# Optimization experiments

Measured on AMD Instinct MI355X. Metric: run time of the kernel, lower is better.

## Reference

```python
import jax, jax.numpy as jnp
import numpy as np

B, S, D, H = 4, 2048, 1024, 16
DK = D // H  # 64


def setup_inputs() -> dict:
    key = jax.random.key(0)
    ks = jax.random.split(key, 11)
    scale = 1.0 / np.sqrt(D)
    inp = {
        "query": jax.random.normal(ks[0], (B, S, D), jnp.float32),
        "key": jax.random.normal(ks[1], (B, S, D), jnp.float32),
        "value": jax.random.normal(ks[2], (B, S, D), jnp.float32),
        "Wq": jax.random.normal(ks[3], (D, D), jnp.float32) * scale,
        "bq": jnp.zeros((D,), jnp.float32),
        "Wk": jax.random.normal(ks[4], (D, D), jnp.float32) * scale,
        "bk": jnp.zeros((D,), jnp.float32),
        "Wv": jax.random.normal(ks[5], (D, D), jnp.float32) * scale,
        "bv": jnp.zeros((D,), jnp.float32),
        "Wo": jax.random.normal(ks[6], (D, D), jnp.float32) * scale,
        "bo": jnp.zeros((D,), jnp.float32),
    }
    return inp


def reference(query, key, value, Wq, bq, Wk, bk, Wv, bv, Wo, bo):
    # Projections: torch Linear computes x @ W.T + b; here W is stored as (in, out)
    def split_heads(x):
        return x.reshape(B, S, H, DK).transpose(0, 2, 1, 3)  # [B,H,S,DK]

    Q = split_heads(query @ Wq + bq)
    K = split_heads(key @ Wk + bk)
    V = split_heads(value @ Wv + bv)

    scores = jnp.einsum("bhqd,bhkd->bhqk", Q, K) / jnp.sqrt(jnp.float32(DK))
    attn = jax.nn.softmax(scores, axis=-1)  # [B,H,S,S]
    ctx = jnp.einsum("bhqk,bhkd->bhqd", attn, V)
    ctx = ctx.transpose(0, 2, 1, 3).reshape(B, S, D)
    return ctx @ Wo + bo
```

## Files before the change

kernel.cpp:

```cpp
#include <hip/hip_runtime.h>
#include <hip/hip_bf16.h>
#include <cstdint>

#define DEV __device__ __forceinline__

typedef __bf16 bf16x8 __attribute__((ext_vector_type(8)));
typedef float f32x4 __attribute__((ext_vector_type(4)));
typedef unsigned short u16;
typedef unsigned short u16x8 __attribute__((ext_vector_type(8)));
typedef unsigned short u16x4 __attribute__((ext_vector_type(4)));

#if defined(__has_builtin) && __has_builtin(__builtin_amdgcn_exp2f)
#define EXP2F(x) __builtin_amdgcn_exp2f(x)
#else
#define EXP2F(x) exp2f(x)
#endif

static constexpr float QSCALE = 0.125f * 1.44269504088896340736f;

DEV u16 f2bf(float f) {
  uint32_t x = __builtin_bit_cast(uint32_t, f);
  x += 0x7fffu + ((x >> 16) & 1u);
  return (u16)(x >> 16);
}

DEV u16x4 pack4(float a, float b, float c, float d) {
  union { __hip_bfloat162 h[2]; u16x4 u; } r;
  r.h[0] = __float22bfloat162_rn(make_float2(a, b));
  r.h[1] = __float22bfloat162_rn(make_float2(c, d));
  return r.u;
}

DEV u16x8 cvt8(const float* p) {
  const float4 v0 = *(const float4*)p;
  const float4 v1 = *(const float4*)(p + 4);
  union { __hip_bfloat162 h[4]; u16x8 u; } r;
  r.h[0] = __float22bfloat162_rn(make_float2(v0.x, v0.y));
  r.h[1] = __float22bfloat162_rn(make_float2(v0.z, v0.w));
  r.h[2] = __float22bfloat162_rn(make_float2(v1.x, v1.y));
  r.h[3] = __float22bfloat162_rn(make_float2(v1.z, v1.w));
  return r.u;
}

DEV f32x4 mfma16(bf16x8 a, bf16x8 b, f32x4 c) {
  return __builtin_amdgcn_mfma_f32_16x16x32_bf16(a, b, c, 0, 0, 0);
}

DEV void gll16(const void* g, const void* l) {
  __builtin_amdgcn_global_load_lds(
      (const __attribute__((address_space(1))) uint32_t*)g,
      (__attribute__((address_space(3))) uint32_t*)l, 16, 0, 0);
}

__global__ __launch_bounds__(256) void cvt_kernel(
    const float* __restrict__ X0, const float* __restrict__ X1,
    const float* __restrict__ X2, u16* __restrict__ Y0,
    u16* __restrict__ Y1, u16* __restrict__ Y2) {
  const float* X = (blockIdx.z == 0) ? X0 : (blockIdx.z == 1) ? X1 : X2;
  u16* Y = (blockIdx.z == 0) ? Y0 : (blockIdx.z == 1) ? Y1 : Y2;
  const size_t i = ((size_t)blockIdx.x * 256 + threadIdx.x) * 8;
  *(u16x8*)(Y + i) = cvt8(X + i);
}

__global__ __launch_bounds__(256) void wtrans_kernel(
    const float* __restrict__ W0, const float* __restrict__ W1,
    const float* __restrict__ W2, const float* __restrict__ W3,
    u16* __restrict__ T0, u16* __restrict__ T1,
    u16* __restrict__ T2, u16* __restrict__ T3) {
  const float* W = (blockIdx.z == 0) ? W0 : (blockIdx.z == 1) ? W1 : (blockIdx.z == 2) ? W2 : W3;
  u16* T = (blockIdx.z == 0) ? T0 : (blockIdx.z == 1) ? T1 : (blockIdx.z == 2) ? T2 : T3;
  __shared__ float tile[32][33];
  const int tid = threadIdx.x;
  const int r = tid >> 3, c0 = (tid & 7) * 4;
  const float4 v = *(const float4*)(W + (size_t)(blockIdx.y * 32 + r) * 1024 + blockIdx.x * 32 + c0);
  tile[r][c0 + 0] = v.x; tile[r][c0 + 1] = v.y; tile[r][c0 + 2] = v.z; tile[r][c0 + 3] = v.w;
  __syncthreads();
  u16x4 o = pack4(tile[c0 + 0][r], tile[c0 + 1][r], tile[c0 + 2][r], tile[c0 + 3][r]);
  *(u16x4*)(T + (size_t)(blockIdx.x * 32 + r) * 1024 + blockIdx.y * 32 + c0) = o;
}

__global__ __launch_bounds__(512) void gemm_qkv_kernel(
    const u16* __restrict__ X0, const u16* __restrict__ X1,
    const u16* __restrict__ X2, const u16* __restrict__ W0t,
    const u16* __restrict__ W1t, const u16* __restrict__ W2t,
    const float* __restrict__ b0, const float* __restrict__ b1,
    const float* __restrict__ b2, u16* __restrict__ O0,
    u16* __restrict__ O1, u16* __restrict__ O2) {
  __shared__ u16 As[128 * 32];
  __shared__ u16 Bs[128 * 32];
  const int z = blockIdx.z;
  const u16* X = (z == 0) ? X0 : (z == 1) ? X1 : X2;
  const u16* Wt = (z == 0) ? W0t : (z == 1) ? W1t : W2t;
  const float* bias = (z == 0) ? b0 : (z == 1) ? b1 : b2;
  u16* O = (z == 0) ? O0 : (z == 1) ? O1 : O2;
  const float scale = (z == 0) ? QSCALE : 1.0f;

  const int tid = threadIdx.x;
  const int w = tid >> 6, lane = tid & 63, ln = lane & 15, quad = lane >> 4;
  const int wm = w >> 1, wn = w & 1;
  const int bm = blockIdx.y * 128, bn = blockIdx.x * 128;

  f32x4 acc[2][4];
#pragma unroll
  for (int i = 0; i < 2; i++)
#pragma unroll
    for (int j = 0; j < 4; j++) acc[i][j] = f32x4{0.f, 0.f, 0.f, 0.f};

  const int lrow = w * 16 + (lane >> 2);
  const u16* ga = X + (size_t)(bm + lrow) * 1024 + (lane & 3) * 8;
  const u16* gb = Wt + (size_t)(bn + lrow) * 1024 + (lane & 3) * 8;
  const u16* lA = As + w * 512;
  const u16* lB = Bs + w * 512;

  for (int kt = 0; kt < 32; ++kt) {
    __syncthreads();
    gll16(ga + kt * 32, lA);
    gll16(gb + kt * 32, lB);
    __syncthreads();

    bf16x8 af[2], bf[4];
#pragma unroll
    for (int i = 0; i < 2; i++) af[i] = *(const bf16x8*)&As[(wm * 32 + i * 16 + ln) * 32 + quad * 8];
#pragma unroll
    for (int j = 0; j < 4; j++) bf[j] = *(const bf16x8*)&Bs[(wn * 64 + j * 16 + ln) * 32 + quad * 8];
#pragma unroll
    for (int i = 0; i < 2; i++)
#pragma unroll
      for (int j = 0; j < 4; j++) acc[i][j] = mfma16(af[i], bf[j], acc[i][j]);
  }

#pragma unroll
  for (int j = 0; j < 4; j++) {
    const int n = bn + wn * 64 + j * 16 + ln;
    const float bv = bias[n];
#pragma unroll
    for (int i = 0; i < 2; i++) {
      const int m0 = bm + wm * 32 + i * 16 + quad * 4;
      const int h = n >> 6, dk = n & 63;
      if (z != 2) {
#pragma unroll
        for (int r = 0; r < 4; r++) {
          const int m = m0 + r, b = m >> 11, s = m & 2047;
          O[((size_t)(b * 16 + h) * 2048 + s) * 64 + dk] = f2bf((acc[i][j][r] + bv) * scale);
        }
      } else {
        const int b = m0 >> 11, s0 = m0 & 2047;
        u16x4 pk = pack4(acc[i][j][0] + bv, acc[i][j][1] + bv,
                         acc[i][j][2] + bv, acc[i][j][3] + bv);
        *(u16x4*)(O + (size_t)((b * 16 + h) * 64 + dk) * 2048 + s0) = pk;
      }
    }
  }
}

__global__ __launch_bounds__(512) void gemm_o_kernel(
    const u16* __restrict__ X, const u16* __restrict__ Wt,
    const float* __restrict__ bias, float* __restrict__ Out) {
  __shared__ u16 As[128 * 32];
  __shared__ u16 Bs[128 * 32];
  const int tid = threadIdx.x;
  const int w = tid >> 6, lane = tid & 63, ln = lane & 15, quad = lane >> 4;
  const int wm = w >> 1, wn = w & 1;
  const int bm = blockIdx.y * 128, bn = blockIdx.x * 128;

  f32x4 acc[2][4];
#pragma unroll
  for (int i = 0; i < 2; i++)
#pragma unroll
    for (int j = 0; j < 4; j++) acc[i][j] = f32x4{0.f, 0.f, 0.f, 0.f};

  const int lrow = w * 16 + (lane >> 2);
  const u16* ga = X + (size_t)(bm + lrow) * 1024 + (lane & 3) * 8;
  const u16* gb = Wt + (size_t)(bn + lrow) * 1024 + (lane & 3) * 8;
  const u16* lA = As + w * 512;
  const u16* lB = Bs + w * 512;

  for (int kt = 0; kt < 32; ++kt) {
    __syncthreads();
    gll16(ga + kt * 32, lA);
    gll16(gb + kt * 32, lB);
    __syncthreads();

    bf16x8 af[2], bf[4];
#pragma unroll
    for (int i = 0; i < 2; i++) af[i] = *(const bf16x8*)&As[(wm * 32 + i * 16 + ln) * 32 + quad * 8];
#pragma unroll
    for (int j = 0; j < 4; j++) bf[j] = *(const bf16x8*)&Bs[(wn * 64 + j * 16 + ln) * 32 + quad * 8];
#pragma unroll
    for (int i = 0; i < 2; i++)
#pragma unroll
      for (int j = 0; j < 4; j++) acc[i][j] = mfma16(af[i], bf[j], acc[i][j]);
  }

#pragma unroll
  for (int j = 0; j < 4; j++) {
    const int n = bn + wn * 64 + j * 16 + ln;
    const float bv = bias[n];
#pragma unroll
    for (int i = 0; i < 2; i++) {
      const int m0 = bm + wm * 32 + i * 16 + quad * 4;
#pragma unroll
      for (int r = 0; r < 4; r++) Out[(size_t)(m0 + r) * 1024 + n] = acc[i][j][r] + bv;
    }
  }
}

__global__ __launch_bounds__(512) void fattn_kernel(
    const u16* __restrict__ Q, const u16* __restrict__ K,
    const u16* __restrict__ V, u16* __restrict__ ctx) {
  __shared__ u16 Ks[64 * 64];
  __shared__ u16 Vs[64 * 64];
  __shared__ u16 Ps[8 * 16 * 64];

  const int tid = threadIdx.x;
  const int w = tid >> 6, lane = tid & 63, ln = lane & 15, quad = lane >> 4;
  const int qt = blockIdx.x, bh = blockIdx.y;
  const size_t base = (size_t)bh * 2048 * 64;

  const int sr = tid >> 3, sc = (tid & 7) * 8;
  const int swc = ((tid & 7) ^ (sr & 7)) * 8;
  const int sw = ln & 7;

  bf16x8 qf[2];
#pragma unroll
  for (int ks = 0; ks < 2; ks++)
    qf[ks] = *(const bf16x8*)(Q + base + (size_t)(qt * 128 + w * 16 + ln) * 64 + ks * 32 + quad * 8);

  f32x4 lv = f32x4{0.f, 0.f, 0.f, 0.f};
  f32x4 accO[4];
#pragma unroll
  for (int d = 0; d < 4; d++) accO[d] = f32x4{0.f, 0.f, 0.f, 0.f};

  u16x8 kr = *(const u16x8*)(K + base + (size_t)sr * 64 + sc);
  u16x8 vr = *(const u16x8*)(V + base + (size_t)sr * 2048 + sc);

  for (int t = 0; t < 32; ++t) {
    __syncthreads();
    *(u16x8*)&Ks[sr * 64 + swc] = kr;
    *(u16x8*)&Vs[sr * 64 + swc] = vr;
    __syncthreads();

    if (t < 31) {
      const int tn = t + 1;
      kr = *(const u16x8*)(K + base + (size_t)(tn * 64 + sr) * 64 + sc);
      vr = *(const u16x8*)(V + base + (size_t)sr * 2048 + tn * 64 + sc);
    }

    f32x4 s[4];
#pragma unroll
    for (int i = 0; i < 4; i++) s[i] = f32x4{0.f, 0.f, 0.f, 0.f};
    __builtin_amdgcn_s_setprio(1);
#pragma unroll
    for (int i = 0; i < 4; i++) {
#pragma unroll
      for (int ks = 0; ks < 2; ks++) {
        const bf16x8 kf = *(const bf16x8*)&Ks[(i * 16 + ln) * 64 + ((4 * ks + quad) ^ sw) * 8];
        s[i] = mfma16(kf, qf[ks], s[i]);
      }
    }
    __builtin_amdgcn_s_setprio(0);

#pragma unroll
    for (int i = 0; i < 4; i++) {
#pragma unroll
      for (int r = 0; r < 4; r++) s[i][r] = EXP2F(s[i][r]);
      lv += s[i];
      *(u16x4*)&Ps[(w * 16 + ln) * 64 +
                   (((2 * i + (quad >> 1)) ^ sw) * 8) + (quad & 1) * 4] =
          pack4(s[i][0], s[i][1], s[i][2], s[i][3]);
    }

    __builtin_amdgcn_s_setprio(1);
#pragma unroll
    for (int ks = 0; ks < 2; ks++) {
      const bf16x8 pf = *(const bf16x8*)&Ps[(w * 16 + ln) * 64 + ((4 * ks + quad) ^ sw) * 8];
#pragma unroll
      for (int dkt = 0; dkt < 4; dkt++) {
        const bf16x8 vf = *(const bf16x8*)&Vs[(dkt * 16 + ln) * 64 + ((4 * ks + quad) ^ sw) * 8];
        accO[dkt] = mfma16(vf, pf, accO[dkt]);
      }
    }
    __builtin_amdgcn_s_setprio(0);
  }

  const int b = bh >> 4, h = bh & 15;
  float l = (lv[0] + lv[1]) + (lv[2] + lv[3]);
  l += __shfl_xor(l, 16, 64);
  l += __shfl_xor(l, 32, 64);
  const float linv = 1.0f / l;
  const int qs = qt * 128 + w * 16 + ln;
#pragma unroll
  for (int dkt = 0; dkt < 4; dkt++) {
    u16x4 pk = pack4(accO[dkt][0] * linv, accO[dkt][1] * linv,
                     accO[dkt][2] * linv, accO[dkt][3] * linv);
    *(u16x4*)(ctx + (size_t)(b * 2048 + qs) * 1024 + h * 64 + dkt * 16 + quad * 4) = pk;
  }
}

extern "C" void kernel_launch(void* const* d_in, const int* in_sizes, int n_in,
                              void* d_out, int out_size, void* d_ws, size_t ws_size,
                              hipStream_t stream) {
  const float* q  = (const float*)d_in[0];
  const float* k  = (const float*)d_in[1];
  const float* v  = (const float*)d_in[2];
  const float* Wq = (const float*)d_in[3];
  const float* bq = (const float*)d_in[4];
  const float* Wk = (const float*)d_in[5];
  const float* bk = (const float*)d_in[6];
  const float* Wv = (const float*)d_in[7];
  const float* bv = (const float*)d_in[8];
  const float* Wo = (const float*)d_in[9];
  const float* bo = (const float*)d_in[10];

  u16* Wtq = (u16*)d_ws;
  u16* Wtk = Wtq + 1024 * 1024;
  u16* Wtv = Wtk + 1024 * 1024;
  u16* Wto = Wtv + 1024 * 1024;
  u16* qb  = Wto + 1024 * 1024;
  u16* kb  = qb + 8192 * 1024;
  u16* vb  = kb + 8192 * 1024;
  u16* Qb  = vb + 8192 * 1024;
  u16* Kb  = Qb + 8192 * 1024;
  u16* Vtb = Kb + 8192 * 1024;
  u16* Cb  = qb;

  cvt_kernel<<<dim3(4096, 1, 3), 256, 0, stream>>>(q, k, v, qb, kb, vb);
  wtrans_kernel<<<dim3(32, 32, 4), 256, 0, stream>>>(Wq, Wk, Wv, Wo, Wtq, Wtk, Wtv, Wto);

  gemm_qkv_kernel<<<dim3(8, 64, 3), 512, 0, stream>>>(
      qb, kb, vb, Wtq, Wtk, Wtv, bq, bk, bv, Qb, Kb, Vtb);

  fattn_kernel<<<dim3(16, 64), 512, 0, stream>>>(Qb, Kb, Vtb, Cb);

  gemm_o_kernel<<<dim3(8, 64), 512, 0, stream>>>(Cb, Wto, bo, (float*)d_out);
}
```

Baseline: 364.3 us.

## Double-buffer LDS tiles in GEMM and attention kernels and remap block order

All three kernels gain double-buffered shared-memory tiles. The next K-tile's loads are issued before computing on the current tile, which removes one __syncthreads per iteration and overlaps global loads with MFMA work. Block indices are also remapped so that consecutive blocks share input rows or heads, aiming for better L2 reuse. LDS use doubles, which may lower occupancy. The single-barrier scheme depends on the next-buffer writes being safely ordered against the previous iteration's reads.

```diff
diff --git a/kernel.cpp b/kernel.cpp
--- a/kernel.cpp
+++ b/kernel.cpp
@@ -86,8 +86,8 @@
     const float* __restrict__ b0, const float* __restrict__ b1,
     const float* __restrict__ b2, u16* __restrict__ O0,
     u16* __restrict__ O1, u16* __restrict__ O2) {
-  __shared__ u16 As[128 * 32];
-  __shared__ u16 Bs[128 * 32];
+  __shared__ u16 As[2][128 * 32];
+  __shared__ u16 Bs[2][128 * 32];
   const int z = blockIdx.z;
   const u16* X = (z == 0) ? X0 : (z == 1) ? X1 : X2;
   const u16* Wt = (z == 0) ? W0t : (z == 1) ? W1t : W2t;
@@ -95,10 +95,14 @@
   u16* O = (z == 0) ? O0 : (z == 1) ? O1 : O2;
   const float scale = (z == 0) ? QSCALE : 1.0f;
 
+  const int nb = blockIdx.y * 8 + blockIdx.x;
+  const int sb = (nb & 7) * 64 + (nb >> 3);
+  const int bxs = sb & 7, bys = sb >> 3;
+
   const int tid = threadIdx.x;
   const int w = tid >> 6, lane = tid & 63, ln = lane & 15, quad = lane >> 4;
   const int wm = w >> 1, wn = w & 1;
-  const int bm = blockIdx.y * 128, bn = blockIdx.x * 128;
+  const int bm = bys * 128, bn = bxs * 128;
 
   f32x4 acc[2][4];
 #pragma unroll
@@ -109,20 +113,29 @@
   const int lrow = w * 16 + (lane >> 2);
   const u16* ga = X + (size_t)(bm + lrow) * 1024 + (lane & 3) * 8;
   const u16* gb = Wt + (size_t)(bn + lrow) * 1024 + (lane & 3) * 8;
-  const u16* lA = As + w * 512;
-  const u16* lB = Bs + w * 512;
-
+  const u16* lA = (const u16*)&As[0][0] + w * 512;
+  const u16* lB = (const u16*)&Bs[0][0] + w * 512;
+
+  gll16(ga, lA);
+  gll16(gb, lB);
+
+#pragma unroll 2
   for (int kt = 0; kt < 32; ++kt) {
     __syncthreads();
-    gll16(ga + kt * 32, lA);
-    gll16(gb + kt * 32, lB);
-    __syncthreads();
+    const int cur = (kt & 1) << 12;
+    if (kt < 31) {
+      const int nxt = 4096 - cur;
+      gll16(ga + (size_t)(kt + 1) * 32, lA + nxt);
+      gll16(gb + (size_t)(kt + 1) * 32, lB + nxt);
+    }
 
     bf16x8 af[2], bf[4];
 #pragma unroll
-    for (int i = 0; i < 2; i++) af[i] = *(const bf16x8*)&As[(wm * 32 + i * 16 + ln) * 32 + quad * 8];
-#pragma unroll
-    for (int j = 0; j < 4; j++) bf[j] = *(const bf16x8*)&Bs[(wn * 64 + j * 16 + ln) * 32 + quad * 8];
+    for (int i = 0; i < 2; i++)
+      af[i] = *(const bf16x8*)&As[0][cur + (wm * 32 + i * 16 + ln) * 32 + quad * 8];
+#pragma unroll
+    for (int j = 0; j < 4; j++)
+      bf[j] = *(const bf16x8*)&Bs[0][cur + (wn * 64 + j * 16 + ln) * 32 + quad * 8];
 #pragma unroll
     for (int i = 0; i < 2; i++)
 #pragma unroll
@@ -156,12 +169,16 @@
 __global__ __launch_bounds__(512) void gemm_o_kernel(
     const u16* __restrict__ X, const u16* __restrict__ Wt,
     const float* __restrict__ bias, float* __restrict__ Out) {
-  __shared__ u16 As[128 * 32];
-  __shared__ u16 Bs[128 * 32];
+  __shared__ u16 As[2][128 * 32];
+  __shared__ u16 Bs[2][128 * 32];
+  const int nb = blockIdx.y * 8 + blockIdx.x;
+  const int sb = (nb & 7) * 64 + (nb >> 3);
+  const int bxs = sb & 7, bys = sb >> 3;
+
   const int tid = threadIdx.x;
   const int w = tid >> 6, lane = tid & 63, ln = lane & 15, quad = lane >> 4;
   const int wm = w >> 1, wn = w & 1;
-  const int bm = blockIdx.y * 128, bn = blockIdx.x * 128;
+  const int bm = bys * 128, bn = bxs * 128;
 
   f32x4 acc[2][4];
 #pragma unroll
@@ -172,20 +189,29 @@
   const int lrow = w * 16 + (lane >> 2);
   const u16* ga = X + (size_t)(bm + lrow) * 1024 + (lane & 3) * 8;
   const u16* gb = Wt + (size_t)(bn + lrow) * 1024 + (lane & 3) * 8;
-  const u16* lA = As + w * 512;
-  const u16* lB = Bs + w * 512;
-
+  const u16* lA = (const u16*)&As[0][0] + w * 512;
+  const u16* lB = (const u16*)&Bs[0][0] + w * 512;
+
+  gll16(ga, lA);
+  gll16(gb, lB);
+
+#pragma unroll 2
   for (int kt = 0; kt < 32; ++kt) {
     __syncthreads();
-    gll16(ga + kt * 32, lA);
-    gll16(gb + kt * 32, lB);
-    __syncthreads();
+    const int cur = (kt & 1) << 12;
+    if (kt < 31) {
+      const int nxt = 4096 - cur;
+      gll16(ga + (size_t)(kt + 1) * 32, lA + nxt);
+      gll16(gb + (size_t)(kt + 1) * 32, lB + nxt);
+    }
 
     bf16x8 af[2], bf[4];
 #pragma unroll
-    for (int i = 0; i < 2; i++) af[i] = *(const bf16x8*)&As[(wm * 32 + i * 16 + ln) * 32 + quad * 8];
-#pragma unroll
-    for (int j = 0; j < 4; j++) bf[j] = *(const bf16x8*)&Bs[(wn * 64 + j * 16 + ln) * 32 + quad * 8];
+    for (int i = 0; i < 2; i++)
+      af[i] = *(const bf16x8*)&As[0][cur + (wm * 32 + i * 16 + ln) * 32 + quad * 8];
+#pragma unroll
+    for (int j = 0; j < 4; j++)
+      bf[j] = *(const bf16x8*)&Bs[0][cur + (wn * 64 + j * 16 + ln) * 32 + quad * 8];
 #pragma unroll
     for (int i = 0; i < 2; i++)
 #pragma unroll
@@ -208,13 +234,16 @@
 __global__ __launch_bounds__(512) void fattn_kernel(
     const u16* __restrict__ Q, const u16* __restrict__ K,
     const u16* __restrict__ V, u16* __restrict__ ctx) {
-  __shared__ u16 Ks[64 * 64];
-  __shared__ u16 Vs[64 * 64];
+  __shared__ u16 Ks[2][64 * 64];
+  __shared__ u16 Vs[2][64 * 64];
   __shared__ u16 Ps[8 * 16 * 64];
 
   const int tid = threadIdx.x;
   const int w = tid >> 6, lane = tid & 63, ln = lane & 15, quad = lane >> 4;
-  const int qt = blockIdx.x, bh = blockIdx.y;
+
+  const int nb = blockIdx.y * 16 + blockIdx.x;
+  const int sb = (nb & 7) * 128 + (nb >> 3);
+  const int qt = sb & 15, bh = sb >> 4;
   const size_t base = (size_t)bh * 2048 * 64;
 
   const int sr = tid >> 3, sc = (tid & 7) * 8;
@@ -231,19 +260,21 @@
 #pragma unroll
   for (int d = 0; d < 4; d++) accO[d] = f32x4{0.f, 0.f, 0.f, 0.f};
 
-  u16x8 kr = *(const u16x8*)(K + base + (size_t)sr * 64 + sc);
-  u16x8 vr = *(const u16x8*)(V + base + (size_t)sr * 2048 + sc);
+  {
+    u16x8 kr = *(const u16x8*)(K + base + (size_t)sr * 64 + sc);
+    u16x8 vr = *(const u16x8*)(V + base + (size_t)sr * 2048 + sc);
+    *(u16x8*)&Ks[0][sr * 64 + swc] = kr;
+    *(u16x8*)&Vs[0][sr * 64 + swc] = vr;
+  }
 
   for (int t = 0; t < 32; ++t) {
     __syncthreads();
-    *(u16x8*)&Ks[sr * 64 + swc] = kr;
-    *(u16x8*)&Vs[sr * 64 + swc] = vr;
-    __syncthreads();
-
+    const int cur = (t & 1) << 12;
+
+    u16x8 krn, vrn;
     if (t < 31) {
-      const int tn = t + 1;
-      kr = *(const u16x8*)(K + base + (size_t)(tn * 64 + sr) * 64 + sc);
-      vr = *(const u16x8*)(V + base + (size_t)sr * 2048 + tn * 64 + sc);
+      krn = *(const u16x8*)(K + base + (size_t)((t + 1) * 64 + sr) * 64 + sc);
+      vrn = *(const u16x8*)(V + base + (size_t)sr * 2048 + (t + 1) * 64 + sc);
     }
 
     f32x4 s[4];
@@ -254,7 +285,7 @@
     for (int i = 0; i < 4; i++) {
 #pragma unroll
       for (int ks = 0; ks < 2; ks++) {
-        const bf16x8 kf = *(const bf16x8*)&Ks[(i * 16 + ln) * 64 + ((4 * ks + quad) ^ sw) * 8];
+        const bf16x8 kf = *(const bf16x8*)&Ks[0][cur + (i * 16 + ln) * 64 + ((4 * ks + quad) ^ sw) * 8];
         s[i] = mfma16(kf, qf[ks], s[i]);
       }
     }
@@ -276,11 +307,17 @@
       const bf16x8 pf = *(const bf16x8*)&Ps[(w * 16 + ln) * 64 + ((4 * ks + quad) ^ sw) * 8];
 #pragma unroll
       for (int dkt = 0; dkt < 4; dkt++) {
-        const bf16x8 vf = *(const bf16x8*)&Vs[(dkt * 16 + ln) * 64 + ((4 * ks + quad) ^ sw) * 8];
+        const bf16x8 vf = *(const bf16x8*)&Vs[0][cur + (dkt * 16 + ln) * 64 + ((4 * ks + quad) ^ sw) * 8];
         accO[dkt] = mfma16(vf, pf, accO[dkt]);
       }
     }
     __builtin_amdgcn_s_setprio(0);
+
+    if (t < 31) {
+      const int nxt = 4096 - cur;
+      *(u16x8*)&Ks[0][nxt + sr * 64 + swc] = krn;
+      *(u16x8*)&Vs[0][nxt + sr * 64 + swc] = vrn;
+    }
   }
 
   const int b = bh >> 4, h = bh & 15;
```

New measurement: 343.6 us. 1.06x faster.
